# Optimization experiments

Measured on AMD Instinct MI355X. Metric: run time of the kernel, lower is better.

The kernel has to match this reference:

```python
import jax, jax.numpy as jnp
import numpy as np

EPS = 1e-6  # config.eps


def setup_inputs() -> dict:
    key = jax.random.key(0)
    k1, k2, k3, k4, k5 = jax.random.split(key, 5)
    B, Lq, Lk, D, Dc = 4, 2048, 4096, 1024, 512
    # scale so Poincare-ball norms stay < 1 (realistic hyperbolic embeddings)
    q = jax.random.normal(k1, (B, Lq, D), dtype=jnp.float32) * 0.01
    k_compressed = jax.random.randint(k2, (B, Lk, Dc), 0, 16, dtype=jnp.int32)  # 4-bit codes
    # up-projection weight, torch Linear layout (out=D, in=Dc)
    W_up = jax.random.normal(k3, (D, Dc), dtype=jnp.float32) / np.sqrt(Dc)
    k_scale = jax.random.uniform(k4, (B, Lk, 1), dtype=jnp.float32) * 0.005
    k_zero = jax.random.uniform(k5, (B, Lk, 1), dtype=jnp.float32) * 16.0
    return {"q": q, "k_compressed": k_compressed, "W_up": W_up,
            "k_scale": k_scale, "k_zero": k_zero}


def reference(q, k_compressed, W_up, k_scale, k_zero):
    # dequantize: (B, Lk, Dc)
    kc = k_scale * (k_compressed.astype(jnp.float32) - k_zero)
    # decompress: (B, Lk, D)  --  Linear(Dc -> D), y = x @ W_up.T
    k = jnp.einsum('bkc,dc->bkd', kc, W_up)

    q_sq = jnp.sum(q * q, axis=-1)   # (B, Lq) raw squared norms
    k_sq = jnp.sum(k * k, axis=-1)   # (B, Lk)

    # ||q - k||^2 via algebraic expansion (avoids (B,Lq,Lk,D) diff tensor)
    cross = jnp.einsum('bqd,bkd->bqk', q, k)                 # (B, Lq, Lk)
    diff_norm_sq = jnp.maximum(q_sq[:, :, None] + k_sq[:, None, :] - 2.0 * cross, 0.0)

    # clamped norms used in the Poincare denominator
    q_cl = jnp.minimum(q_sq, 1.0 - EPS)
    k_cl = jnp.minimum(k_sq, 1.0 - EPS)
    denom = (1.0 - q_cl)[:, :, None] * (1.0 - k_cl)[:, None, :] + EPS

    dist = jnp.arccosh(1.0 + 2.0 * diff_norm_sq / denom)     # (B, Lq, Lk)
    return dist
```

## Files before the change

### kernel.cpp

```cpp
#include <hip/hip_runtime.h>
#include <hip/hip_bf16.h>
#include <stdint.h>

typedef unsigned short u16;

#define B_  4
#define LQ  2048
#define LK  4096
#define D_  1024
#define DC  512
#define EPSF 1e-6f

typedef __bf16 bf16x8 __attribute__((ext_vector_type(8)));
typedef float  f32x4  __attribute__((ext_vector_type(4)));

__device__ __forceinline__ u16 f2bf(float f) {
    uint32_t u = __float_as_uint(f);
    uint32_t r = (u + 0x7FFFu + ((u >> 16) & 1u)) >> 16;
    return (u16)r;
}
__device__ __forceinline__ float bf2f(u16 h) {
    return __uint_as_float(((uint32_t)h) << 16);
}
__device__ __forceinline__ void gload_lds16(const void* g, void* l) {
    __builtin_amdgcn_global_load_lds(
        (const __attribute__((address_space(1))) uint32_t*)g,
        (__attribute__((address_space(3))) uint32_t*)l, 16, 0, 0);
}

#define NB_Q  (B_ * LQ)
#define NB_WT ((D_ / 64) * (DC / 64))
#define NB_WS 4
#define NB_DQ (B_ * LK)

__global__ void prep_all(const float* __restrict__ q, u16* __restrict__ qb,
                         float* __restrict__ qsq,
                         const float* __restrict__ w, u16* __restrict__ wth,
                         u16* __restrict__ wtl, float* __restrict__ partS,
                         const int* __restrict__ kc, const float* __restrict__ scale,
                         const float* __restrict__ zero, u16* __restrict__ codeb,
                         u16* __restrict__ kcb) {
    __shared__ float t[64][65];
    __shared__ float red[4];
    const int bid = blockIdx.x;

    if (bid < NB_Q) {
        int row = bid;
        const float4 v = reinterpret_cast<const float4*>(q + (size_t)row * D_)[threadIdx.x];
        ushort4 o;
        o.x = f2bf(v.x); o.y = f2bf(v.y); o.z = f2bf(v.z); o.w = f2bf(v.w);
        reinterpret_cast<ushort4*>(qb + (size_t)row * D_)[threadIdx.x] = o;
        float s = v.x * v.x + v.y * v.y + v.z * v.z + v.w * v.w;
        #pragma unroll
        for (int off = 32; off; off >>= 1) s += __shfl_down(s, off);
        if ((threadIdx.x & 63) == 0) red[threadIdx.x >> 6] = s;
        __syncthreads();
        if (threadIdx.x == 0) qsq[row] = red[0] + red[1] + red[2] + red[3];
    } else if (bid < NB_Q + NB_WT) {
        int b2 = bid - NB_Q;
        int d0 = (b2 % (D_ / 64)) * 64, c0 = (b2 / (D_ / 64)) * 64;
        int tx = threadIdx.x & 15, ty = threadIdx.x >> 4;
        #pragma unroll
        for (int r = 0; r < 4; r++) {
            float4 v = *reinterpret_cast<const float4*>(&w[(size_t)(d0 + ty + r * 16) * DC + c0 + tx * 4]);
            t[ty + r * 16][tx * 4 + 0] = v.x;
            t[ty + r * 16][tx * 4 + 1] = v.y;
            t[ty + r * 16][tx * 4 + 2] = v.z;
            t[ty + r * 16][tx * 4 + 3] = v.w;
        }
        __syncthreads();
        #pragma unroll
        for (int r = 0; r < 4; r++) {
            int c = c0 + ty + r * 16;
            ushort4 h, l;
            float v0 = t[tx * 4 + 0][ty + r * 16];
            float v1 = t[tx * 4 + 1][ty + r * 16];
            float v2 = t[tx * 4 + 2][ty + r * 16];
            float v3 = t[tx * 4 + 3][ty + r * 16];
            h.x = f2bf(v0); l.x = f2bf(v0 - bf2f(h.x));
            h.y = f2bf(v1); l.y = f2bf(v1 - bf2f(h.y));
            h.z = f2bf(v2); l.z = f2bf(v2 - bf2f(h.z));
            h.w = f2bf(v3); l.w = f2bf(v3 - bf2f(h.w));
            *reinterpret_cast<ushort4*>(&wth[(size_t)c * D_ + d0 + tx * 4]) = h;
            *reinterpret_cast<ushort4*>(&wtl[(size_t)c * D_ + d0 + tx * 4]) = l;
        }
    } else if (bid < NB_Q + NB_WT + NB_WS) {
        int b2 = bid - NB_Q - NB_WT;
        int d = b2 * 256 + threadIdx.x;
        const float4* row = reinterpret_cast<const float4*>(w + (size_t)d * DC);
        float u = 0.f;
        #pragma unroll 8
        for (int i = 0; i < DC / 4; i++) { float4 v = row[i]; u += v.x + v.y + v.z + v.w; }
        float p = u * u;
        #pragma unroll
        for (int off = 32; off; off >>= 1) p += __shfl_down(p, off);
        if ((threadIdx.x & 63) == 0) red[threadIdx.x >> 6] = p;
        __syncthreads();
        if (threadIdx.x == 0) partS[b2] = red[0] + red[1] + red[2] + red[3];
    } else {
        int row = bid - NB_Q - NB_WT - NB_WS;
        float sc = scale[row], z = zero[row];
        int2 v = reinterpret_cast<const int2*>(kc + (size_t)row * DC)[threadIdx.x];
        ushort2 cb, kb;
        cb.x = f2bf((float)v.x);
        cb.y = f2bf((float)v.y);
        kb.x = f2bf(sc * ((float)v.x - z));
        kb.y = f2bf(sc * ((float)v.y - z));
        reinterpret_cast<ushort2*>(codeb + (size_t)row * DC)[threadIdx.x] = cb;
        reinterpret_cast<ushort2*>(kcb + (size_t)row * DC)[threadIdx.x] = kb;
    }
}

__global__ __launch_bounds__(256, 2) void gemm_gq(const u16* __restrict__ Wth,
                                                  const u16* __restrict__ Wtl,
                                                  u16* __restrict__ Gh,
                                                  u16* __restrict__ Gl,
                                                  const u16* __restrict__ Q,
                                                  u16* __restrict__ Cq) {
    __shared__ u16 smem[4][128 * 32];
    const int tid = threadIdx.x;
    const int wid = tid >> 6, lane = tid & 63;
    const int lr = lane & 15, lk = lane >> 4;
    const int wr = wid >> 1, wc = wid & 1;
    const int srow = tid >> 2;
    const int scol = (tid & 3) * 8;

    if (blockIdx.x < 16) {
        const int m0 = (blockIdx.x & 3) * 128, n0 = (blockIdx.x >> 2) * 128;
        const int K = D_;
        f32x4 acc[4][4] = {};
        const size_t gA = (size_t)(m0 + srow) * K + scol;
        const size_t gB = (size_t)(n0 + srow) * K + scol;
        char* ashb = (char*)(&smem[0][0]) + (wid << 10);
        char* aslb = (char*)(&smem[1][0]) + (wid << 10);
        char* bshb = (char*)(&smem[2][0]) + (wid << 10);
        char* bslb = (char*)(&smem[3][0]) + (wid << 10);

        for (int k0 = 0; k0 < K; k0 += 32) {
            gload_lds16(Wth + gA + k0, ashb);
            gload_lds16(Wth + gA + k0 + (size_t)64 * K, ashb + 4096);
            gload_lds16(Wtl + gA + k0, aslb);
            gload_lds16(Wtl + gA + k0 + (size_t)64 * K, aslb + 4096);
            gload_lds16(Wth + gB + k0, bshb);
            gload_lds16(Wth + gB + k0 + (size_t)64 * K, bshb + 4096);
            gload_lds16(Wtl + gB + k0, bslb);
            gload_lds16(Wtl + gB + k0 + (size_t)64 * K, bslb + 4096);
            __syncthreads();
            bf16x8 afh[4], afl[4], bfh[4], bfl[4];
            #pragma unroll
            for (int i = 0; i < 4; i++) {
                int off = (wr * 64 + i * 16 + lr) * 32 + lk * 8;
                afh[i] = *reinterpret_cast<const bf16x8*>(&smem[0][off]);
                afl[i] = *reinterpret_cast<const bf16x8*>(&smem[1][off]);
            }
            #pragma unroll
            for (int j = 0; j < 4; j++) {
                int off = (wc * 64 + j * 16 + lr) * 32 + lk * 8;
                bfh[j] = *reinterpret_cast<const bf16x8*>(&smem[2][off]);
                bfl[j] = *reinterpret_cast<const bf16x8*>(&smem[3][off]);
            }
            #pragma unroll
            for (int i = 0; i < 4; i++)
                #pragma unroll
                for (int j = 0; j < 4; j++) {
                    acc[i][j] = __builtin_amdgcn_mfma_f32_16x16x32_bf16(afh[i], bfh[j], acc[i][j], 0, 0, 0);
                    acc[i][j] = __builtin_amdgcn_mfma_f32_16x16x32_bf16(afh[i], bfl[j], acc[i][j], 0, 0, 0);
                    acc[i][j] = __builtin_amdgcn_mfma_f32_16x16x32_bf16(afl[i], bfh[j], acc[i][j], 0, 0, 0);
                }
            __syncthreads();
        }
        #pragma unroll
        for (int i = 0; i < 4; i++) {
            int row = m0 + wr * 64 + i * 16 + lk * 4;
            #pragma unroll
            for (int j = 0; j < 4; j++) {
                int col = n0 + wc * 64 + j * 16 + lr;
                #pragma unroll
                for (int r = 0; r < 4; r++) {
                    float v = acc[i][j][r];
                    u16 h = f2bf(v);
                    Gh[(size_t)(row + r) * DC + col] = h;
                    Gl[(size_t)(row + r) * DC + col] = f2bf(v - bf2f(h));
                }
            }
        }
    } else {
        const int q2 = blockIdx.x - 16;
        const int m0 = (q2 & 63) * 128, n0 = (q2 >> 6) * 128;
        const int K = D_;
        const int NT = K / 32;
        f32x4 acc[4][4] = {};
        const u16* ag = Q + (size_t)(m0 + srow) * K + scol;
        const u16* bg = Wth + (size_t)(n0 + srow) * K + scol;

        #define STAGE_P(buf, kt) do {                                          \
            char* asb_ = (char*)(&smem[(buf)][0]) + (wid << 10);               \
            char* bsb_ = (char*)(&smem[2 + (buf)][0]) + (wid << 10);           \
            int k0_ = (kt) * 32;                                               \
            gload_lds16(ag + k0_, asb_);                                       \
            gload_lds16(ag + k0_ + (size_t)64 * K, asb_ + 4096);               \
            gload_lds16(bg + k0_, bsb_);                                       \
            gload_lds16(bg + k0_ + (size_t)64 * K, bsb_ + 4096);               \
        } while (0)

        #define COMPUTE_P(buf) do {                                            \
            bf16x8 af[4], bfr[4];                                              \
            _Pragma("unroll")                                                  \
            for (int i = 0; i < 4; i++)                                        \
                af[i] = *reinterpret_cast<const bf16x8*>(                      \
                    &smem[(buf)][(wr * 64 + i * 16 + lr) * 32 + lk * 8]);      \
            _Pragma("unroll")                                                  \
            for (int j = 0; j < 4; j++)                                        \
                bfr[j] = *reinterpret_cast<const bf16x8*>(                     \
                    &smem[2 + (buf)][(wc * 64 + j * 16 + lr) * 32 + lk * 8]);  \
            asm volatile("s_waitcnt lgkmcnt(0)" ::: "memory");                 \
            __builtin_amdgcn_sched_barrier(0);                                 \
            _Pragma("unroll")                                                  \
            for (int i = 0; i < 4; i++)                                        \
                _Pragma("unroll")                                              \
                for (int j = 0; j < 4; j++)                                    \
                    acc[i][j] = __builtin_amdgcn_mfma_f32_16x16x32_bf16(       \
                        af[i], bfr[j], acc[i][j], 0, 0, 0);                    \
        } while (0)

        STAGE_P(0, 0);
        asm volatile("s_waitcnt vmcnt(0)" ::: "memory");
        __builtin_amdgcn_s_barrier();
        int cur = 0;
        for (int t = 0; t < NT - 1; ++t) {
            STAGE_P(cur ^ 1, t + 1);
            COMPUTE_P(cur);
            asm volatile("s_waitcnt vmcnt(0)" ::: "memory");
            __builtin_amdgcn_s_barrier();
            cur ^= 1;
        }
        COMPUTE_P(cur);
        #undef STAGE_P
        #undef COMPUTE_P

        #pragma unroll
        for (int i = 0; i < 4; i++) {
            int row = m0 + wr * 64 + i * 16 + lk * 4;
            #pragma unroll
            for (int j = 0; j < 4; j++) {
                int col = n0 + wc * 64 + j * 16 + lr;
                #pragma unroll
                for (int r = 0; r < 4; r++)
                    Cq[(size_t)(row + r) * DC + col] = f2bf(acc[i][j][r]);
            }
        }
    }
}

__global__ __launch_bounds__(256, 2) void gemm_ksq(const u16* __restrict__ A,
                                                   const u16* __restrict__ Bh,
                                                   const u16* __restrict__ Bl,
                                                   float* __restrict__ part1,
                                                   float* __restrict__ part2) {
    __shared__ u16 As[2][128 * 32];
    __shared__ u16 Bsh[2][128 * 32];
    __shared__ u16 Bsl[2][128 * 32];
    const int tid = threadIdx.x;
    const int wid = tid >> 6, lane = tid & 63;
    const int lr = lane & 15, lk = lane >> 4;
    const int wr = wid >> 1, wc = wid & 1;
    const int m0 = blockIdx.x * 128, n0 = blockIdx.y * 128;
    const int K = DC;
    const int NT = K / 32;

    f32x4 acc[4][4] = {};
    const int srow = tid >> 2;
    const int scol = (tid & 3) * 8;
    const u16* ag = A + (size_t)(m0 + srow) * K + scol;
    const u16* bhg = Bh + (size_t)(n0 + srow) * K + scol;
    const u16* blg = Bl + (size_t)(n0 + srow) * K + scol;

    #define STAGE_K(buf, kt) do {                                          \
        char* asb_  = (char*)(&As[(buf)][0]) + (wid << 10);                \
        char* bshb_ = (char*)(&Bsh[(buf)][0]) + (wid << 10);               \
        char* bslb_ = (char*)(&Bsl[(buf)][0]) + (wid << 10);               \
        int k0_ = (kt) * 32;                                               \
        gload_lds16(ag + k0_, asb_);                                       \
        gload_lds16(ag + k0_ + (size_t)64 * K, asb_ + 4096);               \
        gload_lds16(bhg + k0_, bshb_);                                     \
        gload_lds16(bhg + k0_ + (size_t)64 * K, bshb_ + 4096);             \
        gload_lds16(blg + k0_, bslb_);                                     \
        gload_lds16(blg + k0_ + (size_t)64 * K, bslb_ + 4096);             \
    } while (0)

    #define COMPUTE_K(buf) do {                                            \
        bf16x8 af[4], bh_[4], bl_[4];                                      \
        _Pragma("unroll")                                                  \
        for (int i = 0; i < 4; i++)                                        \
            af[i] = *reinterpret_cast<const bf16x8*>(                      \
                &As[(buf)][(wr * 64 + i * 16 + lr) * 32 + lk * 8]);        \
        _Pragma("unroll")                                                  \
        for (int j = 0; j < 4; j++) {                                      \
            int off = (wc * 64 + j * 16 + lr) * 32 + lk * 8;               \
            bh_[j] = *reinterpret_cast<const bf16x8*>(&Bsh[(buf)][off]);   \
            bl_[j] = *reinterpret_cast<const bf16x8*>(&Bsl[(buf)][off]);   \
        }                                                                  \
        asm volatile("s_waitcnt lgkmcnt(0)" ::: "memory");                 \
        __builtin_amdgcn_sched_barrier(0);                                 \
        _Pragma("unroll")                                                  \
        for (int i = 0; i < 4; i++)                                        \
            _Pragma("unroll")                                              \
            for (int j = 0; j < 4; j++) {                                  \
                acc[i][j] = __builtin_amdgcn_mfma_f32_16x16x32_bf16(       \
                    af[i], bh_[j], acc[i][j], 0, 0, 0);                    \
                acc[i][j] = __builtin_amdgcn_mfma_f32_16x16x32_bf16(       \
                    af[i], bl_[j], acc[i][j], 0, 0, 0);                    \
            }                                                              \
    } while (0)

    STAGE_K(0, 0);
    asm volatile("s_waitcnt vmcnt(0)" ::: "memory");
    __builtin_amdgcn_s_barrier();
    int cur = 0;
    for (int t = 0; t < NT - 1; ++t) {
        STAGE_K(cur ^ 1, t + 1);
        COMPUTE_K(cur);
        asm volatile("s_waitcnt vmcnt(0)" ::: "memory");
        __builtin_amdgcn_s_barrier();
        cur ^= 1;
    }
    COMPUTE_K(cur);
    #undef STAGE_K
    #undef COMPUTE_K

    #pragma unroll
    for (int i = 0; i < 4; i++) {
        #pragma unroll
        for (int r = 0; r < 4; r++) {
            int row = m0 + wr * 64 + i * 16 + lk * 4 + r;
            float p1 = 0.f, p2 = 0.f;
            #pragma unroll
            for (int j = 0; j < 4; j++) {
                int col = n0 + wc * 64 + j * 16 + lr;
                float cg = acc[i][j][r];
                float cd = bf2f(A[(size_t)row * DC + col]);
                p1 = fmaf(cg, cd, p1);
                p2 += cg;
            }
            #pragma unroll
            for (int m = 1; m <= 8; m <<= 1) {
                p1 += __shfl_xor(p1, m);
                p2 += __shfl_xor(p2, m);
            }
            if (lr == 0) {
                size_t idx = (size_t)row * 8 + blockIdx.y * 2 + wc;
                part1[idx] = p1;
                part2[idx] = p2;
            }
        }
    }
}

__global__ __launch_bounds__(256, 2) void gemm_dist2(const u16* __restrict__ Qp,
                                                     const u16* __restrict__ Kc,
                                                     const float* __restrict__ qsq,
                                                     const float* __restrict__ part1,
                                                     const float* __restrict__ part2,
                                                     const float* __restrict__ partS,
                                                     const float* __restrict__ kscale,
                                                     const float* __restrict__ kzero,
                                                     float* __restrict__ out) {
    const int wgid = (blockIdx.x & 7) * 256 + (blockIdx.x >> 3);
    const int bx = wgid & 15, by = (wgid >> 4) & 31, bz = wgid >> 9;

    const u16* A  = Qp + (size_t)bz * LQ * DC;
    const u16* Bt = Kc + (size_t)bz * LK * DC;
    float* O = out + (size_t)bz * LQ * LK;
    const float* qs_ = qsq + bz * LQ;

    __shared__ u16 As[2][128 * 32];
    __shared__ u16 Bs[2][128 * 32];
    __shared__ float kss[128];
    const int tid = threadIdx.x;
    const int wid = tid >> 6, lane = tid & 63;
    const int lr = lane & 15, lk = lane >> 4;
    const int wr = wid >> 1, wc = wid & 1;
    const int m0 = bx * 128, n0 = by * 128;
    const int K = DC;
    const int NT = K / 32;

    if (tid < 128) {
        int gcol = bz * LK + n0 + tid;
        const float4* p1 = reinterpret_cast<const float4*>(part1 + (size_t)gcol * 8);
        const float4* p2 = reinterpret_cast<const float4*>(part2 + (size_t)gcol * 8);
        float4 a0 = p1[0], a1 = p1[1];
        float4 b0 = p2[0], b1 = p2[1];
        float P1 = a0.x + a0.y + a0.z + a0.w + a1.x + a1.y + a1.z + a1.w;
        float P2 = b0.x + b0.y + b0.z + b0.w + b1.x + b1.y + b1.z + b1.w;
        float S = partS[0] + partS[1] + partS[2] + partS[3];
        float sc = kscale[gcol], z = kzero[gcol];
        kss[tid] = sc * sc * (P1 - 2.f * z * P2 + z * z * S);
    }

    f32x4 acc[4][4] = {};
    const int srow = tid >> 2;
    const int scol = (tid & 3) * 8;
    const u16* ag = A + (size_t)(m0 + srow) * K + scol;
    const u16* bg = Bt + (size_t)(n0 + srow) * K + scol;

    #define STAGE_D(buf, kt) do {                                          \
        char* asb_ = (char*)(&As[(buf)][0]) + (wid << 10);                 \
        char* bsb_ = (char*)(&Bs[(buf)][0]) + (wid << 10);                 \
        int k0_ = (kt) * 32;                                               \
        gload_lds16(ag + k0_, asb_);                                       \
        gload_lds16(ag + k0_ + (size_t)64 * K, asb_ + 4096);               \
        gload_lds16(bg + k0_, bsb_);                                       \
        gload_lds16(bg + k0_ + (size_t)64 * K, bsb_ + 4096);               \
    } while (0)

    #define COMPUTE_D(buf) do {                                            \
        bf16x8 af[4], bfr[4];                                              \
        _Pragma("unroll")                                                  \
        for (int i = 0; i < 4; i++)                                        \
            af[i] = *reinterpret_cast<const bf16x8*>(                      \
                &As[(buf)][(wr * 64 + i * 16 + lr) * 32 + lk * 8]);        \
        _Pragma("unroll")                                                  \
        for (int j = 0; j < 4; j++)                                        \
            bfr[j] = *reinterpret_cast<const bf16x8*>(                     \
                &Bs[(buf)][(wc * 64 + j * 16 + lr) * 32 + lk * 8]);        \
        asm volatile("s_waitcnt lgkmcnt(0)" ::: "memory");                 \
        __builtin_amdgcn_sched_barrier(0);                                 \
        _Pragma("unroll")                                                  \
        for (int i = 0; i < 4; i++)                                        \
            _Pragma("unroll")                                              \
            for (int j = 0; j < 4; j++)                                    \
                acc[i][j] = __builtin_amdgcn_mfma_f32_16x16x32_bf16(       \
                    af[i], bfr[j], acc[i][j], 0, 0, 0);                    \
    } while (0)

    STAGE_D(0, 0);
    asm volatile("s_waitcnt vmcnt(0)" ::: "memory");
    __builtin_amdgcn_s_barrier();
    int cur = 0;
    for (int t = 0; t < NT - 1; ++t) {
        STAGE_D(cur ^ 1, t + 1);
        COMPUTE_D(cur);
        asm volatile("s_waitcnt vmcnt(0)" ::: "memory");
        __builtin_amdgcn_s_barrier();
        cur ^= 1;
    }
    COMPUTE_D(cur);
    #undef STAGE_D
    #undef COMPUTE_D

    const float LN2 = 0.69314718055994531f;
    float ksv[4], pkv[4];
    #pragma unroll
    for (int j = 0; j < 4; j++) {
        ksv[j] = kss[wc * 64 + j * 16 + lr];
        pkv[j] = 1.f - fminf(ksv[j], 1.f - EPSF);
    }
    #pragma unroll
    for (int i = 0; i < 4; i++) {
        int row = m0 + wr * 64 + i * 16 + lk * 4;
        #pragma unroll
        for (int r = 0; r < 4; r++) {
            int gr = row + r;
            float qs = qs_[gr];
            float pq = 1.f - fminf(qs, 1.f - EPSF);
            float* orow = O + (size_t)gr * LK + n0 + wc * 64 + lr;
            #pragma unroll
            for (int j = 0; j < 4; j++) {
                float d = fmaxf(fmaf(acc[i][j][r], -2.f, qs + ksv[j]), 0.f);
                float den = fmaf(pq, pkv[j], EPSF);
                float u = (d + d) * __builtin_amdgcn_rcpf(den);
                float s = __builtin_amdgcn_sqrtf(u * (u + 2.f));
                orow[j * 16] = LN2 * __builtin_amdgcn_logf(1.f + u + s);
            }
        }
    }
}

extern "C" void kernel_launch(void* const* d_in, const int* in_sizes, int n_in,
                              void* d_out, int out_size, void* d_ws, size_t ws_size,
                              hipStream_t stream) {
    const float* q      = (const float*)d_in[0];
    const int*   kcmp   = (const int*)d_in[1];
    const float* wup    = (const float*)d_in[2];
    const float* kscale = (const float*)d_in[3];
    const float* kzero  = (const float*)d_in[4];
    float* out = (float*)d_out;

    char* ws = (char*)d_ws;
    u16*   qb    = (u16*)(ws);
    u16*   qp    = (u16*)(ws + 16777216);
    u16*   codeb = (u16*)(ws + 25165824);
    u16*   kcb   = (u16*)(ws + 41943040);
    u16*   wth   = (u16*)(ws + 58720256);
    u16*   wtl   = (u16*)(ws + 59768832);
    u16*   gh    = (u16*)(ws + 60817408);
    u16*   gl    = (u16*)(ws + 61341696);
    float* qsq   = (float*)(ws + 61865984);
    float* part1 = (float*)(ws + 61964288);
    float* part2 = (float*)(ws + 62488576);
    float* partS = (float*)(ws + 63012864);

    prep_all<<<NB_Q + NB_WT + NB_WS + NB_DQ, 256, 0, stream>>>(
        q, qb, qsq, wup, wth, wtl, partS, kcmp, kscale, kzero, codeb, kcb);

    gemm_gq<<<16 + 256, 256, 0, stream>>>(wth, wtl, gh, gl, qb, qp);

    gemm_ksq<<<dim3((B_ * LK) / 128, DC / 128), 256, 0, stream>>>(codeb, gh, gl, part1, part2);

    gemm_dist2<<<2048, 256, 0, stream>>>(qp, kcb, qsq, part1, part2, partS,
                                         kscale, kzero, out);
}
```

Measured before the change: 152.9 us.

## Fold dequant scale/zero into distance epilogue and drop dequantized key buffer

The separately dequantized bf16 key buffer is removed. The main distance GEMM now multiplies projected queries directly against raw code values and applies per-key scale and zero in the epilogue, using per-query row sums of the projected query that gemm_gq emits. The prep kernel processes four rows per block with one wave per row, and gemm_ksq uses a 1D swizzled grid. This cuts prep memory traffic and the extra buffer, at the cost of more epilogue arithmetic and a precision change, since codes are exact in bf16 but the cancellation z*qsum may lose accuracy.

Measured after the change: 158.0 us. 3.3% more time.

```diff
diff --git a/kernel.cpp b/kernel.cpp
--- a/kernel.cpp
+++ b/kernel.cpp
@@ -28,38 +28,42 @@
         (__attribute__((address_space(3))) uint32_t*)l, 16, 0, 0);
 }
 
-#define NB_Q  (B_ * LQ)
-#define NB_WT ((D_ / 64) * (DC / 64))
-#define NB_WS 4
-#define NB_DQ (B_ * LK)
+#define NB_Q2  2048
+#define NB_WT  ((D_ / 64) * (DC / 64))
+#define NB_WS  4
+#define NB_DQ2 4096
 
 __global__ void prep_all(const float* __restrict__ q, u16* __restrict__ qb,
                          float* __restrict__ qsq,
                          const float* __restrict__ w, u16* __restrict__ wth,
                          u16* __restrict__ wtl, float* __restrict__ partS,
-                         const int* __restrict__ kc, const float* __restrict__ scale,
-                         const float* __restrict__ zero, u16* __restrict__ codeb,
-                         u16* __restrict__ kcb) {
+                         const int* __restrict__ kc, u16* __restrict__ codeb) {
     __shared__ float t[64][65];
     __shared__ float red[4];
     const int bid = blockIdx.x;
-
-    if (bid < NB_Q) {
-        int row = bid;
-        const float4 v = reinterpret_cast<const float4*>(q + (size_t)row * D_)[threadIdx.x];
-        ushort4 o;
-        o.x = f2bf(v.x); o.y = f2bf(v.y); o.z = f2bf(v.z); o.w = f2bf(v.w);
-        reinterpret_cast<ushort4*>(qb + (size_t)row * D_)[threadIdx.x] = o;
-        float s = v.x * v.x + v.y * v.y + v.z * v.z + v.w * v.w;
+    const int tid = threadIdx.x;
+
+    if (bid < NB_Q2) {
+        int row = bid * 4 + (tid >> 6);
+        int ln = tid & 63;
+        const float4* qr = reinterpret_cast<const float4*>(q + (size_t)row * D_);
+        ushort4* ob = reinterpret_cast<ushort4*>(qb + (size_t)row * D_);
+        float s = 0.f;
+        #pragma unroll
+        for (int c = 0; c < 4; c++) {
+            float4 v = qr[c * 64 + ln];
+            ushort4 o;
+            o.x = f2bf(v.x); o.y = f2bf(v.y); o.z = f2bf(v.z); o.w = f2bf(v.w);
+            ob[c * 64 + ln] = o;
+            s += v.x * v.x + v.y * v.y + v.z * v.z + v.w * v.w;
+        }
         #pragma unroll
         for (int off = 32; off; off >>= 1) s += __shfl_down(s, off);
-        if ((threadIdx.x & 63) == 0) red[threadIdx.x >> 6] = s;
-        __syncthreads();
-        if (threadIdx.x == 0) qsq[row] = red[0] + red[1] + red[2] + red[3];
-    } else if (bid < NB_Q + NB_WT) {
-        int b2 = bid - NB_Q;
+        if (ln == 0) qsq[row] = s;
+    } else if (bid < NB_Q2 + NB_WT) {
+        int b2 = bid - NB_Q2;
         int d0 = (b2 % (D_ / 64)) * 64, c0 = (b2 / (D_ / 64)) * 64;
-        int tx = threadIdx.x & 15, ty = threadIdx.x >> 4;
+        int tx = tid & 15, ty = tid >> 4;
         #pragma unroll
         for (int r = 0; r < 4; r++) {
             float4 v = *reinterpret_cast<const float4*>(&w[(size_t)(d0 + ty + r * 16) * DC + c0 + tx * 4]);
@@ -84,9 +88,9 @@
             *reinterpret_cast<ushort4*>(&wth[(size_t)c * D_ + d0 + tx * 4]) = h;
             *reinterpret_cast<ushort4*>(&wtl[(size_t)c * D_ + d0 + tx * 4]) = l;
         }
-    } else if (bid < NB_Q + NB_WT + NB_WS) {
-        int b2 = bid - NB_Q - NB_WT;
-        int d = b2 * 256 + threadIdx.x;
+    } else if (bid < NB_Q2 + NB_WT + NB_WS) {
+        int b2 = bid - NB_Q2 - NB_WT;
+        int d = b2 * 256 + tid;
         const float4* row = reinterpret_cast<const float4*>(w + (size_t)d * DC);
         float u = 0.f;
         #pragma unroll 8
@@ -94,20 +98,22 @@
         float p = u * u;
         #pragma unroll
         for (int off = 32; off; off >>= 1) p += __shfl_down(p, off);
-        if ((threadIdx.x & 63) == 0) red[threadIdx.x >> 6] = p;
+        if ((tid & 63) == 0) red[tid >> 6] = p;
         __syncthreads();
-        if (threadIdx.x == 0) partS[b2] = red[0] + red[1] + red[2] + red[3];
+        if (tid == 0) partS[b2] = red[0] + red[1] + red[2] + red[3];
     } else {
-        int row = bid - NB_Q - NB_WT - NB_WS;
-        float sc = scale[row], z = zero[row];
-        int2 v = reinterpret_cast<const int2*>(kc + (size_t)row * DC)[threadIdx.x];
-        ushort2 cb, kb;
-        cb.x = f2bf((float)v.x);
-        cb.y = f2bf((float)v.y);
-        kb.x = f2bf(sc * ((float)v.x - z));
-        kb.y = f2bf(sc * ((float)v.y - z));
-        reinterpret_cast<ushort2*>(codeb + (size_t)row * DC)[threadIdx.x] = cb;
-        reinterpret_cast<ushort2*>(kcb + (size_t)row * DC)[threadIdx.x] = kb;
+        int row = (bid - NB_Q2 - NB_WT - NB_WS) * 4 + (tid >> 6);
+        int ln = tid & 63;
+        const int2* src = reinterpret_cast<const int2*>(kc + (size_t)row * DC);
+        ushort2* dst = reinterpret_cast<ushort2*>(codeb + (size_t)row * DC);
+        #pragma unroll
+        for (int c = 0; c < 4; c++) {
+            int2 v = src[c * 64 + ln];
+            ushort2 cb;
+            cb.x = f2bf((float)v.x);
+            cb.y = f2bf((float)v.y);
+            dst[c * 64 + ln] = cb;
+        }
     }
 }
 
@@ -116,7 +122,8 @@
                                                   u16* __restrict__ Gh,
                                                   u16* __restrict__ Gl,
                                                   const u16* __restrict__ Q,
-                                                  u16* __restrict__ Cq) {
+                                                  u16* __restrict__ Cq,
+                                                  float* __restrict__ qps) {
     __shared__ u16 smem[4][128 * 32];
     const int tid = threadIdx.x;
     const int wid = tid >> 6, lane = tid & 63;
@@ -238,6 +245,7 @@
         #undef STAGE_P
         #undef COMPUTE_P
 
+        const int ntile = q2 >> 6;
         #pragma unroll
         for (int i = 0; i < 4; i++) {
             int row = m0 + wr * 64 + i * 16 + lk * 4;
@@ -247,6 +255,18 @@
                 #pragma unroll
                 for (int r = 0; r < 4; r++)
                     Cq[(size_t)(row + r) * DC + col] = f2bf(acc[i][j][r]);
+            }
+            #pragma unroll
+            for (int r = 0; r < 4; r++) {
+                float p = 0.f;
+                #pragma unroll
+                for (int j = 0; j < 4; j++) p += acc[i][j][r];
+                p += __shfl_xor(p, 1);
+                p += __shfl_xor(p, 2);
+                p += __shfl_xor(p, 4);
+                p += __shfl_xor(p, 8);
+                if (lr == 0)
+                    qps[(size_t)(row + lk * 0 + r) * 8 + ntile * 2 + wc] = p;
             }
         }
     }
@@ -260,11 +280,12 @@
     __shared__ u16 As[2][128 * 32];
     __shared__ u16 Bsh[2][128 * 32];
     __shared__ u16 Bsl[2][128 * 32];
+    const int wg = (blockIdx.x & 7) * 64 + (blockIdx.x >> 3);
+    const int m0 = (wg & 127) * 128, n0 = (wg >> 7) * 128;
     const int tid = threadIdx.x;
     const int wid = tid >> 6, lane = tid & 63;
     const int lr = lane & 15, lk = lane >> 4;
     const int wr = wid >> 1, wc = wid & 1;
-    const int m0 = blockIdx.x * 128, n0 = blockIdx.y * 128;
     const int K = DC;
     const int NT = K / 32;
 
@@ -348,7 +369,7 @@
                 p2 += __shfl_xor(p2, m);
             }
             if (lr == 0) {
-                size_t idx = (size_t)row * 8 + blockIdx.y * 2 + wc;
+                size_t idx = (size_t)row * 8 + (wg >> 7) * 2 + wc;
                 part1[idx] = p1;
                 part2[idx] = p2;
             }
@@ -357,25 +378,26 @@
 }
 
 __global__ __launch_bounds__(256, 2) void gemm_dist2(const u16* __restrict__ Qp,
-                                                     const u16* __restrict__ Kc,
+                                                     const u16* __restrict__ Cd,
                                                      const float* __restrict__ qsq,
                                                      const float* __restrict__ part1,
                                                      const float* __restrict__ part2,
                                                      const float* __restrict__ partS,
                                                      const float* __restrict__ kscale,
                                                      const float* __restrict__ kzero,
+                                                     const float* __restrict__ qps,
                                                      float* __restrict__ out) {
     const int wgid = (blockIdx.x & 7) * 256 + (blockIdx.x >> 3);
     const int bx = wgid & 15, by = (wgid >> 4) & 31, bz = wgid >> 9;
 
     const u16* A  = Qp + (size_t)bz * LQ * DC;
-    const u16* Bt = Kc + (size_t)bz * LK * DC;
+    const u16* Bt = Cd + (size_t)bz * LK * DC;
     float* O = out + (size_t)bz * LQ * LK;
     const float* qs_ = qsq + bz * LQ;
 
     __shared__ u16 As[2][128 * 32];
     __shared__ u16 Bs[2][128 * 32];
-    __shared__ float kss[128];
+    __shared__ float kss[128], ksc[128], ksz[128], qss[128];
     const int tid = threadIdx.x;
     const int wid = tid >> 6, lane = tid & 63;
     const int lr = lane & 15, lk = lane >> 4;
@@ -395,6 +417,14 @@
         float S = partS[0] + partS[1] + partS[2] + partS[3];
         float sc = kscale[gcol], z = kzero[gcol];
         kss[tid] = sc * sc * (P1 - 2.f * z * P2 + z * z * S);
+        ksc[tid] = sc;
+        ksz[tid] = z;
+    } else {
+        int r2 = tid - 128;
+        int grow = bz * LQ + m0 + r2;
+        const float4* p = reinterpret_cast<const float4*>(qps + (size_t)grow * 8);
+        float4 a = p[0], b2 = p[1];
+        qss[r2] = a.x + a.y + a.z + a.w + b2.x + b2.y + b2.z + b2.w;
     }
 
     f32x4 acc[4][4] = {};
@@ -449,24 +479,30 @@
     #undef COMPUTE_D
 
     const float LN2 = 0.69314718055994531f;
-    float ksv[4], pkv[4];
+    float ksv[4], pkv[4], scv[4], zv[4];
     #pragma unroll
     for (int j = 0; j < 4; j++) {
-        ksv[j] = kss[wc * 64 + j * 16 + lr];
+        int c = wc * 64 + j * 16 + lr;
+        ksv[j] = kss[c];
+        scv[j] = ksc[c];
+        zv[j]  = ksz[c];
         pkv[j] = 1.f - fminf(ksv[j], 1.f - EPSF);
     }
     #pragma unroll
     for (int i = 0; i < 4; i++) {
-        int row = m0 + wr * 64 + i * 16 + lk * 4;
+        int rl0 = wr * 64 + i * 16 + lk * 4;
         #pragma unroll
         for (int r = 0; r < 4; r++) {
-            int gr = row + r;
+            int rl = rl0 + r;
+            int gr = m0 + rl;
             float qs = qs_[gr];
+            float qsum = qss[rl];
             float pq = 1.f - fminf(qs, 1.f - EPSF);
             float* orow = O + (size_t)gr * LK + n0 + wc * 64 + lr;
             #pragma unroll
             for (int j = 0; j < 4; j++) {
-                float d = fmaxf(fmaf(acc[i][j][r], -2.f, qs + ksv[j]), 0.f);
+                float cr = acc[i][j][r] - zv[j] * qsum;
+                float d = fmaxf(fmaf(-2.f * scv[j], cr, qs + ksv[j]), 0.f);
                 float den = fmaf(pq, pkv[j], EPSF);
                 float u = (d + d) * __builtin_amdgcn_rcpf(den);
                 float s = __builtin_amdgcn_sqrtf(u * (u + 2.f));
@@ -490,23 +526,23 @@
     u16*   qb    = (u16*)(ws);
     u16*   qp    = (u16*)(ws + 16777216);
     u16*   codeb = (u16*)(ws + 25165824);
-    u16*   kcb   = (u16*)(ws + 41943040);
-    u16*   wth   = (u16*)(ws + 58720256);
-    u16*   wtl   = (u16*)(ws + 59768832);
-    u16*   gh    = (u16*)(ws + 60817408);
-    u16*   gl    = (u16*)(ws + 61341696);
-    float* qsq   = (float*)(ws + 61865984);
-    float* part1 = (float*)(ws + 61964288);
-    float* part2 = (float*)(ws + 62488576);
-    float* partS = (float*)(ws + 63012864);
-
-    prep_all<<<NB_Q + NB_WT + NB_WS + NB_DQ, 256, 0, stream>>>(
-        q, qb, qsq, wup, wth, wtl, partS, kcmp, kscale, kzero, codeb, kcb);
-
-    gemm_gq<<<16 + 256, 256, 0, stream>>>(wth, wtl, gh, gl, qb, qp);
-
-    gemm_ksq<<<dim3((B_ * LK) / 128, DC / 128), 256, 0, stream>>>(codeb, gh, gl, part1, part2);
-
-    gemm_dist2<<<2048, 256, 0, stream>>>(qp, kcb, qsq, part1, part2, partS,
-                                         kscale, kzero, out);
-}
+    u16*   wth   = (u16*)(ws + 41943040);
+    u16*   wtl   = (u16*)(ws + 42991616);
+    u16*   gh    = (u16*)(ws + 44040192);
+    u16*   gl    = (u16*)(ws + 44564480);
+    float* qsq   = (float*)(ws + 45088768);
+    float* part1 = (float*)(ws + 45121536);
+    float* part2 = (float*)(ws + 45645824);
+    float* partS = (float*)(ws + 46170112);
+    float* qps   = (float*)(ws + 46170128);
+
+    prep_all<<<NB_Q2 + NB_WT + NB_WS + NB_DQ2, 256, 0, stream>>>(
+        q, qb, qsq, wup, wth, wtl, partS, kcmp, codeb);
+
+    gemm_gq<<<16 + 256, 256, 0, stream>>>(wth, wtl, gh, gl, qb, qp, qps);
+
+    gemm_ksq<<<512, 256, 0, stream>>>(codeb, gh, gl, part1, part2);
+
+    gemm_dist2<<<2048, 256, 0, stream>>>(qp, codeb, qsq, part1, part2, partS,
+                                         kscale, kzero, qps, out);
+}
```

## Split-K the Gram GEMM, batch prep rows per block, remap ksq block order

Applied to the files above, without the earlier changes.

The W^T W Gram GEMM inside gemm_gq is split four ways along K, giving 64 blocks instead of 16. The fp32 partials go to a new workspace buffer and a new g_reduce kernel sums them and does the hi/lo bf16 split. prep_all now handles four rows per block with one wave each, which removes the LDS reduction and syncthreads and cuts the block count. gemm_ksq uses a 1D grid with a swizzled block order for locality. The cost is an extra kernel launch plus the round trip of the partials through memory.

Measured after the change: 140.9 us. 1.08x faster.

```diff
diff --git a/kernel.cpp b/kernel.cpp
--- a/kernel.cpp
+++ b/kernel.cpp
@@ -28,10 +28,10 @@
         (__attribute__((address_space(3))) uint32_t*)l, 16, 0, 0);
 }
 
-#define NB_Q  (B_ * LQ)
-#define NB_WT ((D_ / 64) * (DC / 64))
-#define NB_WS 4
-#define NB_DQ (B_ * LK)
+#define NB_Q2  2048
+#define NB_WT  ((D_ / 64) * (DC / 64))
+#define NB_WS  4
+#define NB_DQ2 4096
 
 __global__ void prep_all(const float* __restrict__ q, u16* __restrict__ qb,
                          float* __restrict__ qsq,
@@ -43,23 +43,29 @@
     __shared__ float t[64][65];
     __shared__ float red[4];
     const int bid = blockIdx.x;
-
-    if (bid < NB_Q) {
-        int row = bid;
-        const float4 v = reinterpret_cast<const float4*>(q + (size_t)row * D_)[threadIdx.x];
-        ushort4 o;
-        o.x = f2bf(v.x); o.y = f2bf(v.y); o.z = f2bf(v.z); o.w = f2bf(v.w);
-        reinterpret_cast<ushort4*>(qb + (size_t)row * D_)[threadIdx.x] = o;
-        float s = v.x * v.x + v.y * v.y + v.z * v.z + v.w * v.w;
+    const int tid = threadIdx.x;
+
+    if (bid < NB_Q2) {
+        int row = bid * 4 + (tid >> 6);
+        int ln = tid & 63;
+        const float4* qr = reinterpret_cast<const float4*>(q + (size_t)row * D_);
+        ushort4* ob = reinterpret_cast<ushort4*>(qb + (size_t)row * D_);
+        float s = 0.f;
+        #pragma unroll
+        for (int c = 0; c < 4; c++) {
+            float4 v = qr[c * 64 + ln];
+            ushort4 o;
+            o.x = f2bf(v.x); o.y = f2bf(v.y); o.z = f2bf(v.z); o.w = f2bf(v.w);
+            ob[c * 64 + ln] = o;
+            s += v.x * v.x + v.y * v.y + v.z * v.z + v.w * v.w;
+        }
         #pragma unroll
         for (int off = 32; off; off >>= 1) s += __shfl_down(s, off);
-        if ((threadIdx.x & 63) == 0) red[threadIdx.x >> 6] = s;
-        __syncthreads();
-        if (threadIdx.x == 0) qsq[row] = red[0] + red[1] + red[2] + red[3];
-    } else if (bid < NB_Q + NB_WT) {
-        int b2 = bid - NB_Q;
+        if (ln == 0) qsq[row] = s;
+    } else if (bid < NB_Q2 + NB_WT) {
+        int b2 = bid - NB_Q2;
         int d0 = (b2 % (D_ / 64)) * 64, c0 = (b2 / (D_ / 64)) * 64;
-        int tx = threadIdx.x & 15, ty = threadIdx.x >> 4;
+        int tx = tid & 15, ty = tid >> 4;
         #pragma unroll
         for (int r = 0; r < 4; r++) {
             float4 v = *reinterpret_cast<const float4*>(&w[(size_t)(d0 + ty + r * 16) * DC + c0 + tx * 4]);
@@ -84,9 +90,9 @@
             *reinterpret_cast<ushort4*>(&wth[(size_t)c * D_ + d0 + tx * 4]) = h;
             *reinterpret_cast<ushort4*>(&wtl[(size_t)c * D_ + d0 + tx * 4]) = l;
         }
-    } else if (bid < NB_Q + NB_WT + NB_WS) {
-        int b2 = bid - NB_Q - NB_WT;
-        int d = b2 * 256 + threadIdx.x;
+    } else if (bid < NB_Q2 + NB_WT + NB_WS) {
+        int b2 = bid - NB_Q2 - NB_WT;
+        int d = b2 * 256 + tid;
         const float4* row = reinterpret_cast<const float4*>(w + (size_t)d * DC);
         float u = 0.f;
         #pragma unroll 8
@@ -94,27 +100,33 @@
         float p = u * u;
         #pragma unroll
         for (int off = 32; off; off >>= 1) p += __shfl_down(p, off);
-        if ((threadIdx.x & 63) == 0) red[threadIdx.x >> 6] = p;
+        if ((tid & 63) == 0) red[tid >> 6] = p;
         __syncthreads();
-        if (threadIdx.x == 0) partS[b2] = red[0] + red[1] + red[2] + red[3];
+        if (tid == 0) partS[b2] = red[0] + red[1] + red[2] + red[3];
     } else {
-        int row = bid - NB_Q - NB_WT - NB_WS;
+        int row = (bid - NB_Q2 - NB_WT - NB_WS) * 4 + (tid >> 6);
+        int ln = tid & 63;
         float sc = scale[row], z = zero[row];
-        int2 v = reinterpret_cast<const int2*>(kc + (size_t)row * DC)[threadIdx.x];
-        ushort2 cb, kb;
-        cb.x = f2bf((float)v.x);
-        cb.y = f2bf((float)v.y);
-        kb.x = f2bf(sc * ((float)v.x - z));
-        kb.y = f2bf(sc * ((float)v.y - z));
-        reinterpret_cast<ushort2*>(codeb + (size_t)row * DC)[threadIdx.x] = cb;
-        reinterpret_cast<ushort2*>(kcb + (size_t)row * DC)[threadIdx.x] = kb;
+        const int2* src = reinterpret_cast<const int2*>(kc + (size_t)row * DC);
+        ushort2* dc = reinterpret_cast<ushort2*>(codeb + (size_t)row * DC);
+        ushort2* dk = reinterpret_cast<ushort2*>(kcb + (size_t)row * DC);
+        #pragma unroll
+        for (int c = 0; c < 4; c++) {
+            int2 v = src[c * 64 + ln];
+            ushort2 cb, kb;
+            cb.x = f2bf((float)v.x);
+            cb.y = f2bf((float)v.y);
+            kb.x = f2bf(sc * ((float)v.x - z));
+            kb.y = f2bf(sc * ((float)v.y - z));
+            dc[c * 64 + ln] = cb;
+            dk[c * 64 + ln] = kb;
+        }
     }
 }
 
 __global__ __launch_bounds__(256, 2) void gemm_gq(const u16* __restrict__ Wth,
                                                   const u16* __restrict__ Wtl,
-                                                  u16* __restrict__ Gh,
-                                                  u16* __restrict__ Gl,
+                                                  float* __restrict__ gp,
                                                   const u16* __restrict__ Q,
                                                   u16* __restrict__ Cq) {
     __shared__ u16 smem[4][128 * 32];
@@ -125,8 +137,9 @@
     const int srow = tid >> 2;
     const int scol = (tid & 3) * 8;
 
-    if (blockIdx.x < 16) {
-        const int m0 = (blockIdx.x & 3) * 128, n0 = (blockIdx.x >> 2) * 128;
+    if (blockIdx.x < 64) {
+        const int t = blockIdx.x >> 2, s = blockIdx.x & 3;
+        const int m0 = (t & 3) * 128, n0 = (t >> 2) * 128;
         const int K = D_;
         f32x4 acc[4][4] = {};
         const size_t gA = (size_t)(m0 + srow) * K + scol;
@@ -136,7 +149,7 @@
         char* bshb = (char*)(&smem[2][0]) + (wid << 10);
         char* bslb = (char*)(&smem[3][0]) + (wid << 10);
 
-        for (int k0 = 0; k0 < K; k0 += 32) {
+        for (int k0 = s * 256; k0 < s * 256 + 256; k0 += 32) {
             gload_lds16(Wth + gA + k0, ashb);
             gload_lds16(Wth + gA + k0 + (size_t)64 * K, ashb + 4096);
             gload_lds16(Wtl + gA + k0, aslb);
@@ -169,6 +182,7 @@
                 }
             __syncthreads();
         }
+        float* dst = gp + (size_t)s * (DC * DC);
         #pragma unroll
         for (int i = 0; i < 4; i++) {
             int row = m0 + wr * 64 + i * 16 + lk * 4;
@@ -176,16 +190,12 @@
             for (int j = 0; j < 4; j++) {
                 int col = n0 + wc * 64 + j * 16 + lr;
                 #pragma unroll
-                for (int r = 0; r < 4; r++) {
-                    float v = acc[i][j][r];
-                    u16 h = f2bf(v);
-                    Gh[(size_t)(row + r) * DC + col] = h;
-                    Gl[(size_t)(row + r) * DC + col] = f2bf(v - bf2f(h));
-                }
+                for (int r = 0; r < 4; r++)
+                    dst[(size_t)(row + r) * DC + col] = acc[i][j][r];
             }
         }
     } else {
-        const int q2 = blockIdx.x - 16;
+        const int q2 = blockIdx.x - 64;
         const int m0 = (q2 & 63) * 128, n0 = (q2 >> 6) * 128;
         const int K = D_;
         const int NT = K / 32;
@@ -252,6 +262,26 @@
     }
 }
 
+__global__ void g_reduce(const float* __restrict__ gp, u16* __restrict__ Gh,
+                         u16* __restrict__ Gl) {
+    int i = (blockIdx.x * 256 + threadIdx.x) * 4;
+    float4 a = *reinterpret_cast<const float4*>(gp + i);
+    float4 b = *reinterpret_cast<const float4*>(gp + (DC * DC) + i);
+    float4 c = *reinterpret_cast<const float4*>(gp + 2 * (DC * DC) + i);
+    float4 d = *reinterpret_cast<const float4*>(gp + 3 * (DC * DC) + i);
+    float v0 = a.x + b.x + c.x + d.x;
+    float v1 = a.y + b.y + c.y + d.y;
+    float v2 = a.z + b.z + c.z + d.z;
+    float v3 = a.w + b.w + c.w + d.w;
+    ushort4 h, l;
+    h.x = f2bf(v0); l.x = f2bf(v0 - bf2f(h.x));
+    h.y = f2bf(v1); l.y = f2bf(v1 - bf2f(h.y));
+    h.z = f2bf(v2); l.z = f2bf(v2 - bf2f(h.z));
+    h.w = f2bf(v3); l.w = f2bf(v3 - bf2f(h.w));
+    *reinterpret_cast<ushort4*>(Gh + i) = h;
+    *reinterpret_cast<ushort4*>(Gl + i) = l;
+}
+
 __global__ __launch_bounds__(256, 2) void gemm_ksq(const u16* __restrict__ A,
                                                    const u16* __restrict__ Bh,
                                                    const u16* __restrict__ Bl,
@@ -260,11 +290,12 @@
     __shared__ u16 As[2][128 * 32];
     __shared__ u16 Bsh[2][128 * 32];
     __shared__ u16 Bsl[2][128 * 32];
+    const int wg = (blockIdx.x & 7) * 64 + (blockIdx.x >> 3);
+    const int m0 = (wg & 127) * 128, n0 = (wg >> 7) * 128;
     const int tid = threadIdx.x;
     const int wid = tid >> 6, lane = tid & 63;
     const int lr = lane & 15, lk = lane >> 4;
     const int wr = wid >> 1, wc = wid & 1;
-    const int m0 = blockIdx.x * 128, n0 = blockIdx.y * 128;
     const int K = DC;
     const int NT = K / 32;
 
@@ -348,7 +379,7 @@
                 p2 += __shfl_xor(p2, m);
             }
             if (lr == 0) {
-                size_t idx = (size_t)row * 8 + blockIdx.y * 2 + wc;
+                size_t idx = (size_t)row * 8 + (wg >> 7) * 2 + wc;
                 part1[idx] = p1;
                 part2[idx] = p2;
             }
@@ -496,16 +527,19 @@
     u16*   gh    = (u16*)(ws + 60817408);
     u16*   gl    = (u16*)(ws + 61341696);
     float* qsq   = (float*)(ws + 61865984);
-    float* part1 = (float*)(ws + 61964288);
-    float* part2 = (float*)(ws + 62488576);
-    float* partS = (float*)(ws + 63012864);
-
-    prep_all<<<NB_Q + NB_WT + NB_WS + NB_DQ, 256, 0, stream>>>(
+    float* part1 = (float*)(ws + 61898752);
+    float* part2 = (float*)(ws + 62423040);
+    float* partS = (float*)(ws + 62947328);
+    float* gp    = (float*)(ws + 62947344);
+
+    prep_all<<<NB_Q2 + NB_WT + NB_WS + NB_DQ2, 256, 0, stream>>>(
         q, qb, qsq, wup, wth, wtl, partS, kcmp, kscale, kzero, codeb, kcb);
 
-    gemm_gq<<<16 + 256, 256, 0, stream>>>(wth, wtl, gh, gl, qb, qp);
-
-    gemm_ksq<<<dim3((B_ * LK) / 128, DC / 128), 256, 0, stream>>>(codeb, gh, gl, part1, part2);
+    gemm_gq<<<64 + 256, 256, 0, stream>>>(wth, wtl, gp, qb, qp);
+
+    g_reduce<<<DC * DC / 1024, 256, 0, stream>>>(gp, gh, gl);
+
+    gemm_ksq<<<512, 256, 0, stream>>>(codeb, gh, gl, part1, part2);
 
     gemm_dist2<<<2048, 256, 0, stream>>>(qp, kcb, qsq, part1, part2, partS,
                                          kscale, kzero, out);
```
